# Optimization experiments

Measured on AMD Instinct MI355X. Metric: run time of the kernel, lower is better.

## Reference

```python
import jax, jax.numpy as jnp
import numpy as np

D_MODEL = 4096
D_FIBER = 64
D_LATENT = 512
OMEGA = 0.1
B, L = 4, 4096


def cayley(A):
    # Q = (I - A)^{-1} (I + A), batched over leading dim; A is skew-symmetric
    d = A.shape[-1]
    I = jnp.eye(d, dtype=A.dtype)
    return jnp.linalg.solve(I - A, I + A)


def setup_inputs() -> dict:
    key = jax.random.key(0)
    k1, k2, k3, k4, k5 = jax.random.split(key, 5)
    h_t = jax.random.normal(k1, (B, L, D_MODEL), dtype=jnp.float32)
    z0 = jax.random.normal(k2, (B, D_LATENT), dtype=jnp.float32)
    A_raw = jax.random.normal(k3, (B, D_FIBER, D_FIBER), dtype=jnp.float32) * 0.1
    A_u = A_raw - jnp.swapaxes(A_raw, -1, -2)  # skew-symmetric gauge connection
    # frozen projection weights, torch nn.Linear layout: (out_features, in_features)
    W_down = jax.random.normal(k4, (D_FIBER, D_MODEL), dtype=jnp.float32) / np.sqrt(D_MODEL)
    W_up = jax.random.normal(k5, (D_MODEL, D_FIBER), dtype=jnp.float32) / np.sqrt(D_FIBER)
    alpha = jnp.float32(OMEGA)
    return {"h_t": h_t, "z0": z0, "A_u": A_u, "alpha": alpha, "W_down": W_down, "W_up": W_up}


def reference(h_t, z0, A_u, alpha, W_down, W_up):
    # psi_down: (B,L,d_model) @ (d_model,d_fiber)
    h_fiber = jnp.einsum('bld,fd->blf', h_t, W_down)
    Q_u = cayley(A_u)  # (B, d_fiber, d_fiber)
    # h_fiber @ Q_u^T per batch
    h_rot = jnp.einsum('blf,bgf->blg', h_fiber, Q_u)
    delta = h_rot - h_fiber
    h_out = h_t + alpha * jnp.einsum('blf,df->bld', delta, W_up)
    return h_out
```

## Files before the change

### kernel.cpp

```cpp
#include <hip/hip_runtime.h>
#include <hip/hip_bf16.h>

#define D_MODEL 4096
#define NFIB    64
#define NBATCH  4
#define LSEQ    4096
#define TM      16
#define TILES   (LSEQ / TM)

typedef __attribute__((ext_vector_type(4))) float f32x4;
typedef __attribute__((ext_vector_type(8))) short bf16x8;

__device__ __forceinline__ unsigned short f2bf(float f) {
  unsigned int u = __builtin_bit_cast(unsigned int, f);
  u += 0x7FFFu + ((u >> 16) & 1u);
  return (unsigned short)(u >> 16);
}

__device__ __forceinline__ bf16x8 cvt8(f32x4 a, f32x4 b) {
  union { __hip_bfloat162 h2[4]; bf16x8 v; } u;
  u.h2[0] = __float22bfloat162_rn(make_float2(a[0], a[1]));
  u.h2[1] = __float22bfloat162_rn(make_float2(a[2], a[3]));
  u.h2[2] = __float22bfloat162_rn(make_float2(b[0], b[1]));
  u.h2[3] = __float22bfloat162_rn(make_float2(b[2], b[3]));
  return u.v;
}

__global__ __launch_bounds__(256) void cayley_kernel(const float* __restrict__ A,
                                                     float* __restrict__ S) {
  __shared__ float M[64][66];
  __shared__ float R[64][66];
  const int b = blockIdx.x;
  const int tid = threadIdx.x;
  const int k = tid & 63;
  const int g = tid >> 6;
  const float* Ab = A + b * 4096;
#pragma unroll
  for (int ii = 0; ii < 16; ++ii) {
    int i = g * 16 + ii;
    float a = Ab[i * 64 + k];
    M[i][k] = ((i == k) ? 1.0f : 0.0f) - a;
    R[i][k] = 2.0f * a;
  }
  for (int j = 0; j < 64; ++j) {
    __syncthreads();
    float pr  = 1.0f / M[j][j];
    float mjk = M[j][k], rjk = R[j][k];
    float f[16];
#pragma unroll
    for (int ii = 0; ii < 16; ++ii) f[ii] = M[g * 16 + ii][j] * pr;
    __syncthreads();
#pragma unroll
    for (int ii = 0; ii < 16; ++ii) {
      int i = g * 16 + ii;
      if (i != j) { M[i][k] -= f[ii] * mjk; R[i][k] -= f[ii] * rjk; }
    }
  }
  __syncthreads();
  float* Sb = S + b * 4096;
#pragma unroll
  for (int ii = 0; ii < 16; ++ii) {
    int i = g * 16 + ii;
    Sb[i * 64 + k] = R[i][k] / M[i][i];
  }
}

__global__ __launch_bounds__(256) void prep_kernel(const float* __restrict__ Wd,
                                                   const float* __restrict__ Wup,
                                                   const float* __restrict__ S,
                                                   const float* __restrict__ alpha_p,
                                                   unsigned short* __restrict__ Wd2,
                                                   unsigned short* __restrict__ U2) {
  const int blk = blockIdx.x;
  if (blk < 1024) {
    int idx = blk * 256 + threadIdx.x;
    int j    = idx & 7;
    int lane = (idx >> 3) & 63;
    int nf   = (idx >> 9) & 3;
    int ks   = idx >> 11;
    int row = nf * 16 + (lane & 15);
    int col = ks * 32 + (lane >> 4) * 8 + j;
    Wd2[idx] = f2bf(Wd[row * D_MODEL + col]);
  } else {
    __shared__ float Sl[4096];
    const int idx0 = (blk - 1024) * 256;
    const int b = idx0 >> 18;
    const float* Sb = S + b * 4096;
    for (int i = threadIdx.x; i < 1024; i += 256)
      ((f32x4*)Sl)[i] = ((const f32x4*)Sb)[i];
    __syncthreads();
    const int idx = idx0 + threadIdx.x;
    const int j    = idx & 7;
    const int h    = (idx >> 3) & 1;
    const int lane = (idx >> 4) & 63;
    const int nt   = (idx >> 10) & 255;
    const int d = nt * 16 + (lane & 15);
    const int f = h * 32 + (lane >> 4) * 8 + j;
    const float alpha = alpha_p[0];
    const f32x4* wr = (const f32x4*)(Wup + d * 64);
    float s = 0.f;
#pragma unroll
    for (int g4 = 0; g4 < 16; ++g4) {
      f32x4 wv = wr[g4];
      s += wv[0] * Sl[(g4 * 4 + 0) * 64 + f] + wv[1] * Sl[(g4 * 4 + 1) * 64 + f] +
           wv[2] * Sl[(g4 * 4 + 2) * 64 + f] + wv[3] * Sl[(g4 * 4 + 3) * 64 + f];
    }
    U2[idx] = f2bf(alpha * s);
  }
}

__global__ __launch_bounds__(256, 4) void main_kernel(
    const float* __restrict__ H, const unsigned short* __restrict__ Wd2,
    const unsigned short* __restrict__ U2, float* __restrict__ Out) {
  const int blk = blockIdx.x;
  const int b = blk >> 8;
  const int t = blk & 255;
  const int row0 = b * LSEQ + t * TM;

  const int tid = threadIdx.x;
  const int w = tid >> 6, l = tid & 63, lr = l & 15, lq = l >> 4;

  __shared__ float Fp[4][TM][65];
  __shared__ unsigned short Fb[TM][72];

  const float* ha = H + (size_t)(row0 + lr) * D_MODEL + w * 1024 + lq * 8;
  const unsigned short* wb = Wd2 + (size_t)w * 65536 + l * 8;

  f32x4 hb[3][2];
  bf16x8 wf[2][4];
#pragma unroll
  for (int s = 0; s < 3; ++s) {
    hb[s][0] = *(const f32x4*)(ha + s * 32);
    hb[s][1] = *(const f32x4*)(ha + s * 32 + 4);
  }
#pragma unroll
  for (int s = 0; s < 2; ++s)
#pragma unroll
    for (int nf = 0; nf < 4; ++nf)
      wf[s][nf] = *(const bf16x8*)(wb + s * 2048 + nf * 512);

  f32x4 acc[4];
#pragma unroll
  for (int nf = 0; nf < 4; ++nf) acc[nf] = (f32x4){0, 0, 0, 0};

#pragma unroll
  for (int s = 0; s < 32; ++s) {
    bf16x8 afr = cvt8(hb[s % 3][0], hb[s % 3][1]);
#pragma unroll
    for (int nf = 0; nf < 4; ++nf)
      acc[nf] = __builtin_amdgcn_mfma_f32_16x16x32_bf16(afr, wf[s & 1][nf], acc[nf], 0, 0, 0);
    if (s + 3 < 32) {
      hb[s % 3][0] = *(const f32x4*)(ha + (s + 3) * 32);
      hb[s % 3][1] = *(const f32x4*)(ha + (s + 3) * 32 + 4);
    }
    if (s + 2 < 32) {
#pragma unroll
      for (int nf = 0; nf < 4; ++nf)
        wf[s & 1][nf] = *(const bf16x8*)(wb + (s + 2) * 2048 + nf * 512);
    }
  }

#pragma unroll
  for (int nf = 0; nf < 4; ++nf)
#pragma unroll
    for (int rr = 0; rr < 4; ++rr)
      Fp[w][lq * 4 + rr][nf * 16 + lr] = acc[nf][rr];
  __syncthreads();

#pragma unroll
  for (int q = 0; q < 4; ++q) {
    int ee = tid + q * 256;
    int rrow = ee >> 6, ccol = ee & 63;
    float s2 = Fp[0][rrow][ccol] + Fp[1][rrow][ccol] +
               Fp[2][rrow][ccol] + Fp[3][rrow][ccol];
    Fb[rrow][ccol] = f2bf(s2);
  }
  __syncthreads();

  bf16x8 fb0 = *(const bf16x8*)(&Fb[lr][lq * 8]);
  bf16x8 fb1 = *(const bf16x8*)(&Fb[lr][32 + lq * 8]);

  const unsigned short* ub = U2 + (((size_t)b * 256 + w * 64) * 64 + l) * 16;
  const size_t obase = (size_t)(row0 + lr) * D_MODEL + w * 1024 + lq * 4;

  bf16x8 u0r[2], u1r[2];
  f32x4 hr[2];
#pragma unroll
  for (int q = 0; q < 2; ++q) {
    u0r[q] = *(const bf16x8*)(ub + q * 1024);
    u1r[q] = *(const bf16x8*)(ub + q * 1024 + 8);
    hr[q]  = *(const f32x4*)(H + obase + q * 16);
  }

#pragma unroll
  for (int nf = 0; nf < 64; ++nf) {
    f32x4 c = {0, 0, 0, 0};
    c = __builtin_amdgcn_mfma_f32_16x16x32_bf16(u0r[nf & 1], fb0, c, 0, 0, 0);
    c = __builtin_amdgcn_mfma_f32_16x16x32_bf16(u1r[nf & 1], fb1, c, 0, 0, 0);
    f32x4 r = hr[nf & 1];
    if (nf + 2 < 64) {
      u0r[nf & 1] = *(const bf16x8*)(ub + (nf + 2) * 1024);
      u1r[nf & 1] = *(const bf16x8*)(ub + (nf + 2) * 1024 + 8);
      hr[nf & 1]  = *(const f32x4*)(H + obase + (nf + 2) * 16);
    }
    f32x4 v = r + c;
    __builtin_nontemporal_store(v, (f32x4*)(Out + obase + nf * 16));
  }
}

extern "C" void kernel_launch(void* const* d_in, const int* in_sizes, int n_in,
                              void* d_out, int out_size, void* d_ws, size_t ws_size,
                              hipStream_t stream) {
  const float* h_t    = (const float*)d_in[0];
  const float* A_u    = (const float*)d_in[2];
  const float* alpha  = (const float*)d_in[3];
  const float* W_down = (const float*)d_in[4];
  const float* W_up   = (const float*)d_in[5];
  float* out = (float*)d_out;

  char* ws = (char*)d_ws;
  float*          S   = (float*)ws;
  unsigned short* Wd2 = (unsigned short*)(ws + 65536);
  unsigned short* U2  = (unsigned short*)(ws + 65536 + 524288);

  cayley_kernel<<<NBATCH, 256, 0, stream>>>(A_u, S);
  prep_kernel<<<1024 + 4096, 256, 0, stream>>>(W_down, W_up, S, alpha, Wd2, U2);
  main_kernel<<<NBATCH * TILES, 256, 0, stream>>>(h_t, Wd2, U2, out);
}
```

Before: 307.6 us.

## Stage H tiles into LDS via async global_load_lds with 32-row tiles

The main kernel now uses 32-row tiles with 512 threads. H is staged through double-buffered, XOR-swizzled shared memory using global_load_lds, and 8 waves each own a 16x16 output block of the projection, which removes the cross-wave partial-sum reduction. The cayley solve and W_down conversion are merged into one prep launch, and the U prep runs as a separate launch. Output stores change from nontemporal to regular stores, which may add cache pressure. Per-block LDS grows to about 64KB, which may limit occupancy.

Result: slower. 326.8 us (+6.2%).

```diff
diff --git a/kernel.cpp b/kernel.cpp
--- a/kernel.cpp
+++ b/kernel.cpp
@@ -5,8 +5,10 @@
 #define NFIB    64
 #define NBATCH  4
 #define LSEQ    4096
-#define TM      16
-#define TILES   (LSEQ / TM)
+#define TM      32
+#define NTILE   (LSEQ / TM)
+#define KC      256
+#define NCH     (D_MODEL / KC)
 
 typedef __attribute__((ext_vector_type(4))) float f32x4;
 typedef __attribute__((ext_vector_type(8))) short bf16x8;
@@ -26,54 +28,13 @@
   return u.v;
 }
 
-__global__ __launch_bounds__(256) void cayley_kernel(const float* __restrict__ A,
-                                                     float* __restrict__ S) {
-  __shared__ float M[64][66];
-  __shared__ float R[64][66];
-  const int b = blockIdx.x;
-  const int tid = threadIdx.x;
-  const int k = tid & 63;
-  const int g = tid >> 6;
-  const float* Ab = A + b * 4096;
-#pragma unroll
-  for (int ii = 0; ii < 16; ++ii) {
-    int i = g * 16 + ii;
-    float a = Ab[i * 64 + k];
-    M[i][k] = ((i == k) ? 1.0f : 0.0f) - a;
-    R[i][k] = 2.0f * a;
-  }
-  for (int j = 0; j < 64; ++j) {
-    __syncthreads();
-    float pr  = 1.0f / M[j][j];
-    float mjk = M[j][k], rjk = R[j][k];
-    float f[16];
-#pragma unroll
-    for (int ii = 0; ii < 16; ++ii) f[ii] = M[g * 16 + ii][j] * pr;
-    __syncthreads();
-#pragma unroll
-    for (int ii = 0; ii < 16; ++ii) {
-      int i = g * 16 + ii;
-      if (i != j) { M[i][k] -= f[ii] * mjk; R[i][k] -= f[ii] * rjk; }
-    }
-  }
-  __syncthreads();
-  float* Sb = S + b * 4096;
-#pragma unroll
-  for (int ii = 0; ii < 16; ++ii) {
-    int i = g * 16 + ii;
-    Sb[i * 64 + k] = R[i][k] / M[i][i];
-  }
-}
-
-__global__ __launch_bounds__(256) void prep_kernel(const float* __restrict__ Wd,
-                                                   const float* __restrict__ Wup,
-                                                   const float* __restrict__ S,
-                                                   const float* __restrict__ alpha_p,
-                                                   unsigned short* __restrict__ Wd2,
-                                                   unsigned short* __restrict__ U2) {
+__global__ __launch_bounds__(256) void prep1_kernel(const float* __restrict__ A,
+                                                    const float* __restrict__ Wd,
+                                                    float* __restrict__ S,
+                                                    unsigned short* __restrict__ Wd2) {
   const int blk = blockIdx.x;
-  if (blk < 1024) {
-    int idx = blk * 256 + threadIdx.x;
+  if (blk >= NBATCH) {
+    int idx = (blk - NBATCH) * 256 + threadIdx.x;
     int j    = idx & 7;
     int lane = (idx >> 3) & 63;
     int nf   = (idx >> 9) & 3;
@@ -81,107 +42,148 @@
     int row = nf * 16 + (lane & 15);
     int col = ks * 32 + (lane >> 4) * 8 + j;
     Wd2[idx] = f2bf(Wd[row * D_MODEL + col]);
-  } else {
-    __shared__ float Sl[4096];
-    const int idx0 = (blk - 1024) * 256;
-    const int b = idx0 >> 18;
-    const float* Sb = S + b * 4096;
-    for (int i = threadIdx.x; i < 1024; i += 256)
-      ((f32x4*)Sl)[i] = ((const f32x4*)Sb)[i];
+    return;
+  }
+  __shared__ float M[64][66];
+  __shared__ float R[64][66];
+  const int b = blk;
+  const int tid = threadIdx.x;
+  const int k = tid & 63;
+  const int g = tid >> 6;
+  const float* Ab = A + b * 4096;
+#pragma unroll
+  for (int ii = 0; ii < 16; ++ii) {
+    int i = g * 16 + ii;
+    float a = Ab[i * 64 + k];
+    M[i][k] = ((i == k) ? 1.0f : 0.0f) - a;
+    R[i][k] = 2.0f * a;
+  }
+  for (int j = 0; j < 64; ++j) {
     __syncthreads();
-    const int idx = idx0 + threadIdx.x;
-    const int j    = idx & 7;
-    const int h    = (idx >> 3) & 1;
-    const int lane = (idx >> 4) & 63;
-    const int nt   = (idx >> 10) & 255;
-    const int d = nt * 16 + (lane & 15);
-    const int f = h * 32 + (lane >> 4) * 8 + j;
-    const float alpha = alpha_p[0];
-    const f32x4* wr = (const f32x4*)(Wup + d * 64);
-    float s = 0.f;
-#pragma unroll
-    for (int g4 = 0; g4 < 16; ++g4) {
-      f32x4 wv = wr[g4];
-      s += wv[0] * Sl[(g4 * 4 + 0) * 64 + f] + wv[1] * Sl[(g4 * 4 + 1) * 64 + f] +
-           wv[2] * Sl[(g4 * 4 + 2) * 64 + f] + wv[3] * Sl[(g4 * 4 + 3) * 64 + f];
-    }
-    U2[idx] = f2bf(alpha * s);
-  }
-}
-
-__global__ __launch_bounds__(256, 4) void main_kernel(
+    float pr  = 1.0f / M[j][j];
+    float mjk = M[j][k], rjk = R[j][k];
+    float f[16];
+#pragma unroll
+    for (int ii = 0; ii < 16; ++ii) f[ii] = M[g * 16 + ii][j] * pr;
+    __syncthreads();
+#pragma unroll
+    for (int ii = 0; ii < 16; ++ii) {
+      int i = g * 16 + ii;
+      if (i != j) { M[i][k] -= f[ii] * mjk; R[i][k] -= f[ii] * rjk; }
+    }
+  }
+  __syncthreads();
+  float* Sb = S + b * 4096;
+#pragma unroll
+  for (int ii = 0; ii < 16; ++ii) {
+    int i = g * 16 + ii;
+    Sb[i * 64 + k] = R[i][k] / M[i][i];
+  }
+}
+
+__global__ __launch_bounds__(256) void prep_u_kernel(const float* __restrict__ Wup,
+                                                     const float* __restrict__ S,
+                                                     const float* __restrict__ alpha_p,
+                                                     unsigned short* __restrict__ U2) {
+  __shared__ float Sl[4096];
+  const int idx0 = blockIdx.x * 256;
+  const int b = idx0 >> 18;
+  const float* Sb = S + b * 4096;
+  for (int i = threadIdx.x; i < 1024; i += 256)
+    ((f32x4*)Sl)[i] = ((const f32x4*)Sb)[i];
+  __syncthreads();
+  const int idx = idx0 + threadIdx.x;
+  const int j    = idx & 7;
+  const int h    = (idx >> 3) & 1;
+  const int lane = (idx >> 4) & 63;
+  const int nt   = (idx >> 10) & 255;
+  const int d = nt * 16 + (lane & 15);
+  const int f = h * 32 + (lane >> 4) * 8 + j;
+  const float alpha = alpha_p[0];
+  const f32x4* wr = (const f32x4*)(Wup + d * 64);
+  float s = 0.f;
+#pragma unroll
+  for (int g4 = 0; g4 < 16; ++g4) {
+    f32x4 wv = wr[g4];
+    s += wv[0] * Sl[(g4 * 4 + 0) * 64 + f] + wv[1] * Sl[(g4 * 4 + 1) * 64 + f] +
+         wv[2] * Sl[(g4 * 4 + 2) * 64 + f] + wv[3] * Sl[(g4 * 4 + 3) * 64 + f];
+  }
+  U2[idx] = f2bf(alpha * s);
+}
+
+__global__ __launch_bounds__(512, 4) void main_kernel(
     const float* __restrict__ H, const unsigned short* __restrict__ Wd2,
     const unsigned short* __restrict__ U2, float* __restrict__ Out) {
   const int blk = blockIdx.x;
-  const int b = blk >> 8;
-  const int t = blk & 255;
+  const int b = blk >> 7;
+  const int t = blk & 127;
   const int row0 = b * LSEQ + t * TM;
 
   const int tid = threadIdx.x;
   const int w = tid >> 6, l = tid & 63, lr = l & 15, lq = l >> 4;
-
-  __shared__ float Fp[4][TM][65];
-  __shared__ unsigned short Fb[TM][72];
-
-  const float* ha = H + (size_t)(row0 + lr) * D_MODEL + w * 1024 + lq * 8;
-  const unsigned short* wb = Wd2 + (size_t)w * 65536 + l * 8;
-
-  f32x4 hb[3][2];
-  bf16x8 wf[2][4];
-#pragma unroll
-  for (int s = 0; s < 3; ++s) {
-    hb[s][0] = *(const f32x4*)(ha + s * 32);
-    hb[s][1] = *(const f32x4*)(ha + s * 32 + 4);
-  }
-#pragma unroll
-  for (int s = 0; s < 2; ++s)
-#pragma unroll
-    for (int nf = 0; nf < 4; ++nf)
-      wf[s][nf] = *(const bf16x8*)(wb + s * 2048 + nf * 512);
-
-  f32x4 acc[4];
-#pragma unroll
-  for (int nf = 0; nf < 4; ++nf) acc[nf] = (f32x4){0, 0, 0, 0};
-
-#pragma unroll
-  for (int s = 0; s < 32; ++s) {
-    bf16x8 afr = cvt8(hb[s % 3][0], hb[s % 3][1]);
-#pragma unroll
-    for (int nf = 0; nf < 4; ++nf)
-      acc[nf] = __builtin_amdgcn_mfma_f32_16x16x32_bf16(afr, wf[s & 1][nf], acc[nf], 0, 0, 0);
-    if (s + 3 < 32) {
-      hb[s % 3][0] = *(const f32x4*)(ha + (s + 3) * 32);
-      hb[s % 3][1] = *(const f32x4*)(ha + (s + 3) * 32 + 4);
-    }
-    if (s + 2 < 32) {
-#pragma unroll
-      for (int nf = 0; nf < 4; ++nf)
-        wf[s & 1][nf] = *(const bf16x8*)(wb + (s + 2) * 2048 + nf * 512);
-    }
-  }
-
-#pragma unroll
-  for (int nf = 0; nf < 4; ++nf)
-#pragma unroll
-    for (int rr = 0; rr < 4; ++rr)
-      Fp[w][lq * 4 + rr][nf * 16 + lr] = acc[nf][rr];
+  const int wgT = w >> 2, wgF = w & 3;
+
+  __shared__ float Hs[2 * TM * KC];
+  __shared__ __attribute__((aligned(16))) unsigned short Fb[TM][72];
+
+  const char* hb = (const char*)(H + (size_t)row0 * D_MODEL);
+  auto lds3 = (__attribute__((address_space(3))) char*)Hs;
+
+#define STAGE(KCH, BUF)                                                          \
+  {                                                                              \
+    _Pragma("unroll")                                                            \
+    for (int q = 0; q < 4; ++q) {                                                \
+      int i = (w << 2) + q;                                                      \
+      const char* g = hb + (size_t)i * 16384 + (size_t)(KCH) * 1024 +            \
+                      ((l * 16) ^ ((i & 7) << 4));                               \
+      __builtin_amdgcn_global_load_lds(                                          \
+          (const __attribute__((address_space(1))) void*)g,                      \
+          (__attribute__((address_space(3))) void*)(lds3 + (BUF) * 32768 +       \
+                                                    i * 1024),                   \
+          16, 0, 0);                                                             \
+    }                                                                            \
+  }
+
+  f32x4 acc = {0, 0, 0, 0};
+  const int rowA = wgT * 16 + lr;
+  const int abase = rowA * 1024;
+  const int axor = (rowA & 7) << 4;
+
+  STAGE(0, 0);
+  for (int k = 0; k < NCH; ++k) {
+    const int buf = k & 1;
+    if (k + 1 < NCH) {
+      STAGE(k + 1, buf ^ 1);
+      asm volatile("s_waitcnt vmcnt(4)" ::: "memory");
+    } else {
+      asm volatile("s_waitcnt vmcnt(0)" ::: "memory");
+    }
+    __builtin_amdgcn_s_barrier();
+    __builtin_amdgcn_sched_barrier(0);
+
+#pragma unroll
+    for (int s = 0; s < 8; ++s) {
+      const int coff = s * 128 + lq * 32;
+      f32x4 h0 = *(const f32x4*)((const char*)Hs + buf * 32768 + abase + ((coff) ^ axor));
+      f32x4 h1 = *(const f32x4*)((const char*)Hs + buf * 32768 + abase + ((coff + 16) ^ axor));
+      bf16x8 bfr = *(const bf16x8*)(Wd2 + (((size_t)(k * 8 + s) * 4 + wgF) * 64 + l) * 8);
+      acc = __builtin_amdgcn_mfma_f32_16x16x32_bf16(cvt8(h0, h1), bfr, acc, 0, 0, 0);
+    }
+    __builtin_amdgcn_s_barrier();
+  }
+#undef STAGE
+
+#pragma unroll
+  for (int rr = 0; rr < 4; ++rr)
+    Fb[wgT * 16 + lq * 4 + rr][wgF * 16 + lr] = f2bf(acc[rr]);
   __syncthreads();
 
-#pragma unroll
-  for (int q = 0; q < 4; ++q) {
-    int ee = tid + q * 256;
-    int rrow = ee >> 6, ccol = ee & 63;
-    float s2 = Fp[0][rrow][ccol] + Fp[1][rrow][ccol] +
-               Fp[2][rrow][ccol] + Fp[3][rrow][ccol];
-    Fb[rrow][ccol] = f2bf(s2);
-  }
-  __syncthreads();
-
-  bf16x8 fb0 = *(const bf16x8*)(&Fb[lr][lq * 8]);
-  bf16x8 fb1 = *(const bf16x8*)(&Fb[lr][32 + lq * 8]);
-
-  const unsigned short* ub = U2 + (((size_t)b * 256 + w * 64) * 64 + l) * 16;
-  const size_t obase = (size_t)(row0 + lr) * D_MODEL + w * 1024 + lq * 4;
+  const int tg = w >> 2, dq = w & 3;
+  bf16x8 fb0 = *(const bf16x8*)(&Fb[tg * 16 + lr][lq * 8]);
+  bf16x8 fb1 = *(const bf16x8*)(&Fb[tg * 16 + lr][32 + lq * 8]);
+
+  const unsigned short* ub = U2 + (((size_t)b * 256 + dq * 64) * 64 + l) * 16;
+  const size_t obase = (size_t)(row0 + tg * 16 + lr) * D_MODEL + dq * 1024 + lq * 4;
 
   bf16x8 u0r[2], u1r[2];
   f32x4 hr[2];
@@ -203,8 +205,7 @@
       u1r[nf & 1] = *(const bf16x8*)(ub + (nf + 2) * 1024 + 8);
       hr[nf & 1]  = *(const f32x4*)(H + obase + (nf + 2) * 16);
     }
-    f32x4 v = r + c;
-    __builtin_nontemporal_store(v, (f32x4*)(Out + obase + nf * 16));
+    *(f32x4*)(Out + obase + nf * 16) = r + c;
   }
 }
 
@@ -223,7 +224,7 @@
   unsigned short* Wd2 = (unsigned short*)(ws + 65536);
   unsigned short* U2  = (unsigned short*)(ws + 65536 + 524288);
 
-  cayley_kernel<<<NBATCH, 256, 0, stream>>>(A_u, S);
-  prep_kernel<<<1024 + 4096, 256, 0, stream>>>(W_down, W_up, S, alpha, Wd2, U2);
-  main_kernel<<<NBATCH * TILES, 256, 0, stream>>>(h_t, Wd2, U2, out);
-}
+  prep1_kernel<<<NBATCH + 1024, 256, 0, stream>>>(A_u, W_down, S, Wd2);
+  prep_u_kernel<<<4096, 256, 0, stream>>>(W_up, S, alpha, U2);
+  main_kernel<<<NBATCH * NTILE, 512, 0, stream>>>(h_t, Wd2, U2, out);
+}
```
